# Performance work log

Measured on AMD Instinct MI355X. Metric: run time of the kernel, lower is better.

## Reference

```python
import jax, jax.numpy as jnp
import numpy as np

B, N_NUC, N_UP, N_DOWN = 512, 16, 32, 32
N_ELEC = N_UP + N_DOWN            # 64 electrons
F = 8                             # edge feature dim (Gaussian RBF envelopes)
D = N_NUC * F                     # embedding_dim = 128 (positional electron embeddings)
L = 3                             # n_interactions
N_ATOM_TYPES = 4


def _rbf(diff):
    # diff: [..., 3] -> [..., F]; Gaussian RBF features of the interparticle distance
    d = jnp.sqrt(jnp.sum(diff * diff, axis=-1) + 1e-12)
    mu = jnp.linspace(0.0, 4.0, F, dtype=diff.dtype)
    return jnp.exp(-(d[..., None] - mu) ** 2)


def setup_inputs() -> dict:
    key = jax.random.key(0)
    ks = jax.random.split(key, 9)
    r = 2.0 * jax.random.normal(ks[0], (B, N_ELEC, 3), dtype=jnp.float32)
    R = 2.0 * jax.random.normal(ks[1], (B, N_NUC, 3), dtype=jnp.float32)
    atom_types = jax.random.randint(ks[2], (N_NUC,), 0, N_ATOM_TYPES)
    embed_table = 0.1 * jax.random.normal(ks[3], (N_ATOM_TYPES, D), dtype=jnp.float32)
    we_same = 0.1 * jax.random.normal(ks[4], (L, F, D), dtype=jnp.float32)
    we_anti = 0.1 * jax.random.normal(ks[5], (L, F, D), dtype=jnp.float32)
    we_ne = 0.1 * jax.random.normal(ks[6], (L, F, D), dtype=jnp.float32)
    w_up = 0.05 * jax.random.normal(ks[7], (L, 4 * D, D), dtype=jnp.float32)
    b_up = jnp.zeros((L, D), dtype=jnp.float32)
    return {
        'r': r, 'R': R, 'embed_table': embed_table,
        'we_same': we_same, 'we_anti': we_anti, 'we_ne': we_ne,
        'w_up': w_up, 'b_up': b_up, 'atom_types': atom_types,
    }


def reference(r, R, embed_table, we_same, we_anti, we_ne, w_up, b_up, atom_types):
    # --- molecular graph edge construction (pairwise differences + edge features) ---
    ee_feat = _rbf(r[:, :, None, :] - r[:, None, :, :])   # [B, e, e, F]
    ne_feat = _rbf(r[:, :, None, :] - R[:, None, :, :])   # [B, e, n, F]

    spin = jnp.arange(N_ELEC) >= N_UP
    eye = jnp.eye(N_ELEC, dtype=bool)
    same_m = ((spin[:, None] == spin[None, :]) & ~eye).astype(ee_feat.dtype)  # no self-interaction
    anti_m = (spin[:, None] != spin[None, :]).astype(ee_feat.dtype)
    feat_same = ee_feat * same_m[None, :, :, None]
    feat_anti = ee_feat * anti_m[None, :, :, None]

    # --- node factory: positional electron embeddings (dense scatter of ne features == reshape) ---
    x = ne_feat.reshape(ne_feat.shape[0], N_ELEC, N_NUC * F)  # [B, e, D]
    y = embed_table[atom_types]                               # [n, D] nuclei embeddings

    # --- message-passing layers ---
    for l in range(L):
        # messages = Linear(edge_feats) * sender embedding, summed over senders per receiver;
        # contract sender axis first to keep intermediates at [B, e, F, D]
        t_s = jnp.einsum('bijf,bjd->bifd', feat_same, x)
        z_s = jnp.einsum('bifd,fd->bid', t_s, we_same[l])
        t_a = jnp.einsum('bijf,bjd->bifd', feat_anti, x)
        z_a = jnp.einsum('bifd,fd->bid', t_a, we_anti[l])
        t_n = jnp.einsum('binf,nd->bifd', ne_feat, y)
        z_n = jnp.einsum('bifd,fd->bid', t_n, we_ne[l])
        upd = jnp.concatenate([x, z_s, z_a, z_n], axis=-1)    # [B, e, 4D]
        x = x + jnp.tanh(upd @ w_up[l] + b_up[l])
    return x  # final electron embeddings [B, N_ELEC, D]
```

## Files before the change

### kernel.cpp

```cpp
#include <hip/hip_runtime.h>


typedef unsigned short u16;
typedef unsigned int u32;
typedef __attribute__((ext_vector_type(8))) short short8;
typedef __attribute__((ext_vector_type(4))) float f32x4;
typedef __attribute__((ext_vector_type(4))) u32 u32x4;
typedef _Float16 h2 __attribute__((ext_vector_type(2)));

__device__ __forceinline__ u16 f2h(float f){ return __builtin_bit_cast(u16, (_Float16)f); }
__device__ __forceinline__ float h2f(u16 a){ return (float)__builtin_bit_cast(_Float16, a); }

__device__ __forceinline__ short8 rbf8(float dd){
  short8 a;
#pragma unroll
  for (int f = 0; f < 8; f++){
    float u = dd - (4.0f/7.0f)*(float)f;
    a[f] = (short)f2h(__expf(-u*u));
  }
  return a;
}

__global__ __launch_bounds__(256) void gnn_prep(
    const float* __restrict__ w_up, const float* __restrict__ we_ne,
    const float* __restrict__ embed, const int* __restrict__ atypes,
    u16* __restrict__ wsegs){
  __shared__ u16 lw[16384];
  const int blk = blockIdx.x;
  const int l = blk / 5, seg = blk % 5;
  const int tid = threadIdx.x;
  if (seg < 4){
    const float* src = w_up + (l*512 + seg*128)*128;
#pragma unroll
    for (int mm = 0; mm < 16; mm++){
      int idx = mm*1024 + tid*4;
      float4 v = *(const float4*)(src + idx);
      lw[idx+0] = f2h(v.x); lw[idx+1] = f2h(v.y);
      lw[idx+2] = f2h(v.z); lw[idx+3] = f2h(v.w);
    }
  } else {
#pragma unroll
    for (int mm = 0; mm < 16; mm++){
      int idx = mm*1024 + tid*4;
      int k = idx >> 7, dout = idx & 127;
      int n = k >> 3, f = k & 7;
      float4 ye = *(const float4*)(embed + atypes[n]*128 + dout);
      float4 wn = *(const float4*)(we_ne + (l*8 + f)*128 + dout);
      lw[idx+0] = f2h(ye.x*wn.x); lw[idx+1] = f2h(ye.y*wn.y);
      lw[idx+2] = f2h(ye.z*wn.z); lw[idx+3] = f2h(ye.w*wn.w);
    }
  }
  __syncthreads();
  u16* dst = wsegs + blk*16384;
  const int col = tid & 15, q = (tid >> 4) & 3;
#pragma unroll
  for (int m = 0; m < 8; m++){
    int slot = m*4 + (tid >> 6);
    int c = slot >> 3, nt = slot & 7;
    int kbase = c*32 + q*8;
    int dout = nt*16 + col;
    short8 vv;
#pragma unroll
    for (int jj = 0; jj < 8; jj++) vv[jj] = (short)lw[(kbase+jj)*128 + dout];
    *(short8*)(dst + m*2048 + tid*8) = vv;
  }
}

__global__ __launch_bounds__(256, 2) void gnn_main(
    const float* __restrict__ r_g, const float* __restrict__ R_g,
    const float* __restrict__ weS_g, const float* __restrict__ weA_g,
    const float* __restrict__ bup_g,
    const u16* __restrict__ wsegs,
    float* __restrict__ out)
{
  extern __shared__ __attribute__((aligned(16))) u16 lds[];
  u16* const wb  = lds;
  u16* const xb  = lds + 16384;
  u16* const zst = lds + 25088;

  const int tid  = threadIdx.x;
  const int lane = tid & 63;
  const int w    = tid >> 6;
  const int b    = blockIdx.x;
  const int col  = lane & 15;
  const int q    = lane >> 4;
  const int i0   = w * 16;
  const int sp   = w >> 1;
  const int mrow = i0 + col;
  const int loff = (q*16 + col) * 8;

  u32x4 stg[8];
  auto stg_ld = [&](const u16* src){
#pragma unroll
    for (int m = 0; m < 8; m++) stg[m] = *(const u32x4*)(src + m*2048 + tid*8);
  };
  auto stg_st = [&](u16* dst){
#pragma unroll
    for (int m = 0; m < 8; m++) *(u32x4*)(dst + m*2048 + tid*8) = stg[m];
  };
  auto gemm_seg = [&](const u16* wbuf, const u16* arows, f32x4* acc){
#pragma unroll
    for (int c = 0; c < 4; c++){
      short8 a = *(const short8*)(arows + mrow*136 + c*32 + (q<<3));
#pragma unroll
      for (int nt = 0; nt < 8; nt++){
        short8 bf = *(const short8*)(wbuf + c*4096 + nt*512 + loff);
        acc[nt] = __builtin_amdgcn_mfma_f32_16x16x32_f16(a, bf, acc[nt], 0, 0, 0);
      }
    }
  };

  short8 aS[8], aA[8];
  float dN[4];
  {
    float* rs = (float*)zst;
    float* Rs = rs + 256;
    if (tid < 64){
#pragma unroll
      for (int k = 0; k < 3; k++) rs[tid*4+k] = r_g[(b*64+tid)*3 + k];
    } else if (tid < 80){
      int n = tid - 64;
#pragma unroll
      for (int k = 0; k < 3; k++) Rs[n*4+k] = R_g[(b*16+n)*3 + k];
    }
    __syncthreads();
    {
      float x0 = rs[mrow*4], x1 = rs[mrow*4+1], x2 = rs[mrow*4+2];
#pragma unroll
      for (int c = 0; c < 8; c++){
        int j = 32*sp + 4*c + q;
        float dx = x0-rs[j*4], dy = x1-rs[j*4+1], dz = x2-rs[j*4+2];
        float dd = sqrtf(dx*dx + dy*dy + dz*dz + 1e-12f);
        aS[c] = rbf8(dd);
        if (j == mrow) aS[c] = (short8)0;
        j = 32*(1-sp) + 4*c + q;
        dx = x0-rs[j*4]; dy = x1-rs[j*4+1]; dz = x2-rs[j*4+2];
        aA[c] = rbf8(sqrtf(dx*dx + dy*dy + dz*dz + 1e-12f));
      }
#pragma unroll
      for (int c = 0; c < 4; c++){
        int n = 4*c + q;
        float dx = x0-Rs[n*4], dy = x1-Rs[n*4+1], dz = x2-Rs[n*4+2];
        dN[c] = sqrtf(dx*dx + dy*dy + dz*dz + 1e-12f);
      }
    }
    {
      int i = tid >> 2, nb = (tid & 3)*4;
      float y0 = rs[i*4], y1 = rs[i*4+1], y2 = rs[i*4+2];
#pragma unroll
      for (int nn = 0; nn < 4; nn++){
        int n = nb + nn;
        float dx = y0-Rs[n*4], dy = y1-Rs[n*4+1], dz = y2-Rs[n*4+2];
        float dd = sqrtf(dx*dx + dy*dy + dz*dz + 1e-12f);
        *(short8*)&xb[i*136 + n*8] = rbf8(dd);
      }
    }
    stg_ld(wsegs + 0);
    stg_st(wb);
    __syncthreads();
  }

  f32x4 xr[8];
#pragma unroll
  for (int nt = 0; nt < 8; nt++)
#pragma unroll
    for (int rr = 0; rr < 4; rr++)
      xr[nt][rr] = h2f(xb[(i0 + q*4 + rr)*136 + nt*16 + col]);

  const f32x4 vzero = {0.f, 0.f, 0.f, 0.f};

#pragma unroll 1
  for (int l = 0; l < 3; l++){
    const u16* slab = wsegs + l*81920;

    float bupr[8];
#pragma unroll
    for (int nt = 0; nt < 8; nt++) bupr[nt] = bup_g[l*128 + nt*16 + col];

    f32x4 upd[8];
#pragma unroll
    for (int nt = 0; nt < 8; nt++) upd[nt] = vzero;

    auto zpass = [&](int pass){
      const float* weX = pass ? weA_g : weS_g;
      const int jb0 = pass ? 32*(1-sp) : 32*sp;
      const short8* aF = pass ? aA : aS;
      f32x4 zacc[8];
#pragma unroll
      for (int nt = 0; nt < 8; nt++) zacc[nt] = vzero;
#pragma unroll
      for (int nt = 0; nt < 8; nt++){
        h2 wp[4];
#pragma unroll
        for (int p = 0; p < 4; p++){
          h2 t;
          t[0] = (_Float16)weX[(l*8 + 2*p  )*128 + nt*16 + col];
          t[1] = (_Float16)weX[(l*8 + 2*p+1)*128 + nt*16 + col];
          wp[p] = t;
        }
        u16 xv[8];
#pragma unroll
        for (int c = 0; c < 8; c++) xv[c] = xb[(jb0 + 4*c + q)*136 + nt*16 + col];
#pragma unroll
        for (int c = 0; c < 8; c++){
          _Float16 xh = __builtin_bit_cast(_Float16, xv[c]);
          h2 xd; xd[0] = xh; xd[1] = xh;
          u32x4 bu;
#pragma unroll
          for (int p = 0; p < 4; p++)
            bu[p] = __builtin_bit_cast(u32, (h2)(xd * wp[p]));
          short8 bf = __builtin_bit_cast(short8, bu);
          zacc[nt] = __builtin_amdgcn_mfma_f32_16x16x32_f16(aF[c], bf, zacc[nt], 0, 0, 0);
        }
      }
#pragma unroll
      for (int nt = 0; nt < 8; nt++)
#pragma unroll
        for (int rr = 0; rr < 4; rr++)
          zst[(i0 + q*4 + rr)*136 + nt*16 + col] = f2h(zacc[nt][rr]);
    };

    stg_ld(slab + 1*16384);
    zpass(0);
    gemm_seg(wb, xb, upd);
    __syncthreads();  stg_st(wb);  __syncthreads();
    stg_ld(slab + 2*16384);
    gemm_seg(wb, zst, upd);
    __syncthreads();  stg_st(wb);  __syncthreads();
    stg_ld(slab + 4*16384);
    zpass(1);
    gemm_seg(wb, zst, upd);
    __syncthreads();  stg_st(wb);  __syncthreads();
    stg_ld(slab + 3*16384);
    {
      f32x4 zn[8];
#pragma unroll
      for (int nt = 0; nt < 8; nt++) zn[nt] = vzero;
#pragma unroll
      for (int c = 0; c < 4; c++){
        short8 a = rbf8(dN[c]);
#pragma unroll
        for (int nt = 0; nt < 8; nt++){
          short8 bf = *(const short8*)(wb + c*4096 + nt*512 + loff);
          zn[nt] = __builtin_amdgcn_mfma_f32_16x16x32_f16(a, bf, zn[nt], 0, 0, 0);
        }
      }
#pragma unroll
      for (int nt = 0; nt < 8; nt++)
#pragma unroll
        for (int rr = 0; rr < 4; rr++)
          zst[(i0 + q*4 + rr)*136 + nt*16 + col] = f2h(zn[nt][rr]);
    }
    __syncthreads();  stg_st(wb);  __syncthreads();
    if (l < 2) stg_ld(slab + 81920);
    gemm_seg(wb, zst, upd);
#pragma unroll
    for (int nt = 0; nt < 8; nt++){
#pragma unroll
      for (int rr = 0; rr < 4; rr++){
        float v = upd[nt][rr] + bupr[nt];
        float e = __expf(2.0f * v);
        float th = 1.0f - 2.0f * __builtin_amdgcn_rcpf(e + 1.0f);
        xr[nt][rr] += th;
      }
    }
    if (l < 2){
#pragma unroll
      for (int nt = 0; nt < 8; nt++)
#pragma unroll
        for (int rr = 0; rr < 4; rr++)
          xb[(i0 + q*4 + rr)*136 + nt*16 + col] = f2h(xr[nt][rr]);
      __syncthreads();  stg_st(wb);  __syncthreads();
    } else {
#pragma unroll
      for (int nt = 0; nt < 8; nt++)
#pragma unroll
        for (int rr = 0; rr < 4; rr++)
          out[(b*64 + i0 + q*4 + rr)*128 + nt*16 + col] = xr[nt][rr];
    }
  }
}

extern "C" void kernel_launch(void* const* d_in, const int* in_sizes, int n_in,
                              void* d_out, int out_size, void* d_ws, size_t ws_size,
                              hipStream_t stream){
  const float* r     = (const float*)d_in[0];
  const float* R     = (const float*)d_in[1];
  const float* embed = (const float*)d_in[2];
  const float* weS   = (const float*)d_in[3];
  const float* weA   = (const float*)d_in[4];
  const float* weN   = (const float*)d_in[5];
  const float* wup   = (const float*)d_in[6];
  const float* bup   = (const float*)d_in[7];
  const int* atyp    = (const int*)d_in[8];

  u16* wsegs = (u16*)d_ws;

  (void)hipFuncSetAttribute((const void*)gnn_main,
                            hipFuncAttributeMaxDynamicSharedMemorySize, 67584);
  gnn_prep<<<15, 256, 0, stream>>>(wup, weN, embed, atyp, wsegs);
  gnn_main<<<512, 256, 67584, stream>>>(r, R, weS, weA, bup, wsegs, (float*)d_out);
}
```

Before: 134.5 us.

## Split each row tile's output columns across two waves using 512-thread blocks

Doubles the block to 512 threads (8 waves). Each pair of waves now shares a 16-row tile and each wave computes half of the 128 output columns (4 of 8 n-tiles). This halves the accumulator and staging registers per wave and spreads each batch element's work over more waves to improve latency hiding. A barrier is added after the anti-spin z pass because z rows are now written by two waves. The cost is more block-wide synchronisation, and the edge-feature A fragments are recomputed redundantly in both waves of each pair.

Result: slower. 183.2 us (+36.2%).

```diff
diff --git a/kernel.cpp b/kernel.cpp
--- a/kernel.cpp
+++ b/kernel.cpp
@@ -66,7 +66,7 @@
   }
 }
 
-__global__ __launch_bounds__(256, 2) void gnn_main(
+__global__ __launch_bounds__(512, 4) void gnn_main(
     const float* __restrict__ r_g, const float* __restrict__ R_g,
     const float* __restrict__ weS_g, const float* __restrict__ weA_g,
     const float* __restrict__ bup_g,
@@ -81,30 +81,33 @@
   const int tid  = threadIdx.x;
   const int lane = tid & 63;
   const int w    = tid >> 6;
+  const int wq   = w >> 1;
+  const int wc   = w & 1;
   const int b    = blockIdx.x;
   const int col  = lane & 15;
   const int q    = lane >> 4;
-  const int i0   = w * 16;
-  const int sp   = w >> 1;
+  const int i0   = wq * 16;
+  const int sp   = wq >> 1;
   const int mrow = i0 + col;
   const int loff = (q*16 + col) * 8;
-
-  u32x4 stg[8];
+  const int ntb  = wc * 4;
+
+  u32x4 stg[4];
   auto stg_ld = [&](const u16* src){
 #pragma unroll
-    for (int m = 0; m < 8; m++) stg[m] = *(const u32x4*)(src + m*2048 + tid*8);
+    for (int m = 0; m < 4; m++) stg[m] = *(const u32x4*)(src + m*4096 + tid*8);
   };
   auto stg_st = [&](u16* dst){
 #pragma unroll
-    for (int m = 0; m < 8; m++) *(u32x4*)(dst + m*2048 + tid*8) = stg[m];
+    for (int m = 0; m < 4; m++) *(u32x4*)(dst + m*4096 + tid*8) = stg[m];
   };
   auto gemm_seg = [&](const u16* wbuf, const u16* arows, f32x4* acc){
 #pragma unroll
     for (int c = 0; c < 4; c++){
       short8 a = *(const short8*)(arows + mrow*136 + c*32 + (q<<3));
 #pragma unroll
-      for (int nt = 0; nt < 8; nt++){
-        short8 bf = *(const short8*)(wbuf + c*4096 + nt*512 + loff);
+      for (int nt = 0; nt < 4; nt++){
+        short8 bf = *(const short8*)(wbuf + c*4096 + (ntb+nt)*512 + loff);
         acc[nt] = __builtin_amdgcn_mfma_f32_16x16x32_f16(a, bf, acc[nt], 0, 0, 0);
       }
     }
@@ -145,10 +148,10 @@
       }
     }
     {
-      int i = tid >> 2, nb = (tid & 3)*4;
+      int i = tid >> 3, nb = (tid & 7)*2;
       float y0 = rs[i*4], y1 = rs[i*4+1], y2 = rs[i*4+2];
 #pragma unroll
-      for (int nn = 0; nn < 4; nn++){
+      for (int nn = 0; nn < 2; nn++){
         int n = nb + nn;
         float dx = y0-Rs[n*4], dy = y1-Rs[n*4+1], dz = y2-Rs[n*4+2];
         float dd = sqrtf(dx*dx + dy*dy + dz*dz + 1e-12f);
@@ -160,12 +163,12 @@
     __syncthreads();
   }
 
-  f32x4 xr[8];
-#pragma unroll
-  for (int nt = 0; nt < 8; nt++)
+  f32x4 xr[4];
+#pragma unroll
+  for (int nt = 0; nt < 4; nt++)
 #pragma unroll
     for (int rr = 0; rr < 4; rr++)
-      xr[nt][rr] = h2f(xb[(i0 + q*4 + rr)*136 + nt*16 + col]);
+      xr[nt][rr] = h2f(xb[(i0 + q*4 + rr)*136 + (ntb+nt)*16 + col]);
 
   const f32x4 vzero = {0.f, 0.f, 0.f, 0.f};
 
@@ -173,34 +176,35 @@
   for (int l = 0; l < 3; l++){
     const u16* slab = wsegs + l*81920;
 
-    float bupr[8];
-#pragma unroll
-    for (int nt = 0; nt < 8; nt++) bupr[nt] = bup_g[l*128 + nt*16 + col];
-
-    f32x4 upd[8];
-#pragma unroll
-    for (int nt = 0; nt < 8; nt++) upd[nt] = vzero;
+    float bupr[4];
+#pragma unroll
+    for (int nt = 0; nt < 4; nt++) bupr[nt] = bup_g[l*128 + (ntb+nt)*16 + col];
+
+    f32x4 upd[4];
+#pragma unroll
+    for (int nt = 0; nt < 4; nt++) upd[nt] = vzero;
 
     auto zpass = [&](int pass){
       const float* weX = pass ? weA_g : weS_g;
       const int jb0 = pass ? 32*(1-sp) : 32*sp;
       const short8* aF = pass ? aA : aS;
-      f32x4 zacc[8];
-#pragma unroll
-      for (int nt = 0; nt < 8; nt++) zacc[nt] = vzero;
-#pragma unroll
-      for (int nt = 0; nt < 8; nt++){
+      f32x4 zacc[4];
+#pragma unroll
+      for (int nt = 0; nt < 4; nt++) zacc[nt] = vzero;
+#pragma unroll
+      for (int nt = 0; nt < 4; nt++){
+        const int ntg = ntb + nt;
         h2 wp[4];
 #pragma unroll
         for (int p = 0; p < 4; p++){
           h2 t;
-          t[0] = (_Float16)weX[(l*8 + 2*p  )*128 + nt*16 + col];
-          t[1] = (_Float16)weX[(l*8 + 2*p+1)*128 + nt*16 + col];
+          t[0] = (_Float16)weX[(l*8 + 2*p  )*128 + ntg*16 + col];
+          t[1] = (_Float16)weX[(l*8 + 2*p+1)*128 + ntg*16 + col];
           wp[p] = t;
         }
         u16 xv[8];
 #pragma unroll
-        for (int c = 0; c < 8; c++) xv[c] = xb[(jb0 + 4*c + q)*136 + nt*16 + col];
+        for (int c = 0; c < 8; c++) xv[c] = xb[(jb0 + 4*c + q)*136 + ntg*16 + col];
 #pragma unroll
         for (int c = 0; c < 8; c++){
           _Float16 xh = __builtin_bit_cast(_Float16, xv[c]);
@@ -214,10 +218,10 @@
         }
       }
 #pragma unroll
-      for (int nt = 0; nt < 8; nt++)
+      for (int nt = 0; nt < 4; nt++)
 #pragma unroll
         for (int rr = 0; rr < 4; rr++)
-          zst[(i0 + q*4 + rr)*136 + nt*16 + col] = f2h(zacc[nt][rr]);
+          zst[(i0 + q*4 + rr)*136 + (ntb+nt)*16 + col] = f2h(zacc[nt][rr]);
     };
 
     stg_ld(slab + 1*16384);
@@ -229,33 +233,34 @@
     __syncthreads();  stg_st(wb);  __syncthreads();
     stg_ld(slab + 4*16384);
     zpass(1);
+    __syncthreads();
     gemm_seg(wb, zst, upd);
     __syncthreads();  stg_st(wb);  __syncthreads();
     stg_ld(slab + 3*16384);
     {
-      f32x4 zn[8];
-#pragma unroll
-      for (int nt = 0; nt < 8; nt++) zn[nt] = vzero;
+      f32x4 zn[4];
+#pragma unroll
+      for (int nt = 0; nt < 4; nt++) zn[nt] = vzero;
 #pragma unroll
       for (int c = 0; c < 4; c++){
         short8 a = rbf8(dN[c]);
 #pragma unroll
-        for (int nt = 0; nt < 8; nt++){
-          short8 bf = *(const short8*)(wb + c*4096 + nt*512 + loff);
+        for (int nt = 0; nt < 4; nt++){
+          short8 bf = *(const short8*)(wb + c*4096 + (ntb+nt)*512 + loff);
           zn[nt] = __builtin_amdgcn_mfma_f32_16x16x32_f16(a, bf, zn[nt], 0, 0, 0);
         }
       }
 #pragma unroll
-      for (int nt = 0; nt < 8; nt++)
+      for (int nt = 0; nt < 4; nt++)
 #pragma unroll
         for (int rr = 0; rr < 4; rr++)
-          zst[(i0 + q*4 + rr)*136 + nt*16 + col] = f2h(zn[nt][rr]);
+          zst[(i0 + q*4 + rr)*136 + (ntb+nt)*16 + col] = f2h(zn[nt][rr]);
     }
     __syncthreads();  stg_st(wb);  __syncthreads();
     if (l < 2) stg_ld(slab + 81920);
     gemm_seg(wb, zst, upd);
 #pragma unroll
-    for (int nt = 0; nt < 8; nt++){
+    for (int nt = 0; nt < 4; nt++){
 #pragma unroll
       for (int rr = 0; rr < 4; rr++){
         float v = upd[nt][rr] + bupr[nt];
@@ -266,17 +271,17 @@
     }
     if (l < 2){
 #pragma unroll
-      for (int nt = 0; nt < 8; nt++)
+      for (int nt = 0; nt < 4; nt++)
 #pragma unroll
         for (int rr = 0; rr < 4; rr++)
-          xb[(i0 + q*4 + rr)*136 + nt*16 + col] = f2h(xr[nt][rr]);
+          xb[(i0 + q*4 + rr)*136 + (ntb+nt)*16 + col] = f2h(xr[nt][rr]);
       __syncthreads();  stg_st(wb);  __syncthreads();
     } else {
 #pragma unroll
-      for (int nt = 0; nt < 8; nt++)
+      for (int nt = 0; nt < 4; nt++)
 #pragma unroll
         for (int rr = 0; rr < 4; rr++)
-          out[(b*64 + i0 + q*4 + rr)*128 + nt*16 + col] = xr[nt][rr];
+          out[(b*64 + i0 + q*4 + rr)*128 + (ntb+nt)*16 + col] = xr[nt][rr];
     }
   }
 }
@@ -299,5 +304,5 @@
   (void)hipFuncSetAttribute((const void*)gnn_main,
                             hipFuncAttributeMaxDynamicSharedMemorySize, 67584);
   gnn_prep<<<15, 256, 0, stream>>>(wup, weN, embed, atyp, wsegs);
-  gnn_main<<<512, 256, 67584, stream>>>(r, R, weS, weA, bup, wsegs, (float*)d_out);
+  gnn_main<<<512, 512, 67584, stream>>>(r, R, weS, weA, bup, wsegs, (float*)d_out);
 }
```

## Read weight fragments directly from global memory instead of LDS staging

Applied to the files above, without the earlier changes.

Removes the register-staged copy of each packed weight segment into LDS and the paired barriers around it. The MFMA B-fragments are now loaded straight from the global workspace, which every block shares and so should mostly hit in L2. This roughly halves the dynamic LDS footprint and cuts the number of __syncthreads per layer. The trade-off is that global-load latency now sits directly in the MFMA inner loops, with no explicit prefetch to hide it.

Measured after the change: 142.5 us. +6.0%, slower.

```diff
diff --git a/kernel.cpp b/kernel.cpp
--- a/kernel.cpp
+++ b/kernel.cpp
@@ -74,9 +74,10 @@
     float* __restrict__ out)
 {
   extern __shared__ __attribute__((aligned(16))) u16 lds[];
-  u16* const wb  = lds;
-  u16* const xb  = lds + 16384;
-  u16* const zst = lds + 25088;
+  u16* const xb  = lds;
+  u16* const zst = lds + 8704;
+  float* const rs = (float*)(lds + 17408);
+  float* const Rs = rs + 256;
 
   const int tid  = threadIdx.x;
   const int lane = tid & 63;
@@ -89,22 +90,13 @@
   const int mrow = i0 + col;
   const int loff = (q*16 + col) * 8;
 
-  u32x4 stg[8];
-  auto stg_ld = [&](const u16* src){
-#pragma unroll
-    for (int m = 0; m < 8; m++) stg[m] = *(const u32x4*)(src + m*2048 + tid*8);
-  };
-  auto stg_st = [&](u16* dst){
-#pragma unroll
-    for (int m = 0; m < 8; m++) *(u32x4*)(dst + m*2048 + tid*8) = stg[m];
-  };
-  auto gemm_seg = [&](const u16* wbuf, const u16* arows, f32x4* acc){
+  auto gemm_seg = [&](const u16* wseg_g, const u16* arows, f32x4* acc){
 #pragma unroll
     for (int c = 0; c < 4; c++){
       short8 a = *(const short8*)(arows + mrow*136 + c*32 + (q<<3));
 #pragma unroll
       for (int nt = 0; nt < 8; nt++){
-        short8 bf = *(const short8*)(wbuf + c*4096 + nt*512 + loff);
+        short8 bf = *(const short8*)(wseg_g + c*4096 + nt*512 + loff);
         acc[nt] = __builtin_amdgcn_mfma_f32_16x16x32_f16(a, bf, acc[nt], 0, 0, 0);
       }
     }
@@ -113,8 +105,6 @@
   short8 aS[8], aA[8];
   float dN[4];
   {
-    float* rs = (float*)zst;
-    float* Rs = rs + 256;
     if (tid < 64){
 #pragma unroll
       for (int k = 0; k < 3; k++) rs[tid*4+k] = r_g[(b*64+tid)*3 + k];
@@ -155,8 +145,6 @@
         *(short8*)&xb[i*136 + n*8] = rbf8(dd);
       }
     }
-    stg_ld(wsegs + 0);
-    stg_st(wb);
     __syncthreads();
   }
 
@@ -172,10 +160,6 @@
 #pragma unroll 1
   for (int l = 0; l < 3; l++){
     const u16* slab = wsegs + l*81920;
-
-    float bupr[8];
-#pragma unroll
-    for (int nt = 0; nt < 8; nt++) bupr[nt] = bup_g[l*128 + nt*16 + col];
 
     f32x4 upd[8];
 #pragma unroll
@@ -220,19 +204,13 @@
           zst[(i0 + q*4 + rr)*136 + nt*16 + col] = f2h(zacc[nt][rr]);
     };
 
-    stg_ld(slab + 1*16384);
     zpass(0);
-    gemm_seg(wb, xb, upd);
-    __syncthreads();  stg_st(wb);  __syncthreads();
-    stg_ld(slab + 2*16384);
-    gemm_seg(wb, zst, upd);
-    __syncthreads();  stg_st(wb);  __syncthreads();
-    stg_ld(slab + 4*16384);
+    gemm_seg(slab + 0*16384, xb,  upd);
+    gemm_seg(slab + 1*16384, zst, upd);
     zpass(1);
-    gemm_seg(wb, zst, upd);
-    __syncthreads();  stg_st(wb);  __syncthreads();
-    stg_ld(slab + 3*16384);
-    {
+    gemm_seg(slab + 2*16384, zst, upd);
+    {
+      const u16* yseg = slab + 4*16384;
       f32x4 zn[8];
 #pragma unroll
       for (int nt = 0; nt < 8; nt++) zn[nt] = vzero;
@@ -241,7 +219,7 @@
         short8 a = rbf8(dN[c]);
 #pragma unroll
         for (int nt = 0; nt < 8; nt++){
-          short8 bf = *(const short8*)(wb + c*4096 + nt*512 + loff);
+          short8 bf = *(const short8*)(yseg + c*4096 + nt*512 + loff);
           zn[nt] = __builtin_amdgcn_mfma_f32_16x16x32_f16(a, bf, zn[nt], 0, 0, 0);
         }
       }
@@ -251,17 +229,21 @@
         for (int rr = 0; rr < 4; rr++)
           zst[(i0 + q*4 + rr)*136 + nt*16 + col] = f2h(zn[nt][rr]);
     }
-    __syncthreads();  stg_st(wb);  __syncthreads();
-    if (l < 2) stg_ld(slab + 81920);
-    gemm_seg(wb, zst, upd);
-#pragma unroll
-    for (int nt = 0; nt < 8; nt++){
-#pragma unroll
-      for (int rr = 0; rr < 4; rr++){
-        float v = upd[nt][rr] + bupr[nt];
-        float e = __expf(2.0f * v);
-        float th = 1.0f - 2.0f * __builtin_amdgcn_rcpf(e + 1.0f);
-        xr[nt][rr] += th;
+    gemm_seg(slab + 3*16384, zst, upd);
+
+    {
+      float bupr[8];
+#pragma unroll
+      for (int nt = 0; nt < 8; nt++) bupr[nt] = bup_g[l*128 + nt*16 + col];
+#pragma unroll
+      for (int nt = 0; nt < 8; nt++){
+#pragma unroll
+        for (int rr = 0; rr < 4; rr++){
+          float v = upd[nt][rr] + bupr[nt];
+          float e = __expf(2.0f * v);
+          float th = 1.0f - 2.0f * __builtin_amdgcn_rcpf(e + 1.0f);
+          xr[nt][rr] += th;
+        }
       }
     }
     if (l < 2){
@@ -270,7 +252,7 @@
 #pragma unroll
         for (int rr = 0; rr < 4; rr++)
           xb[(i0 + q*4 + rr)*136 + nt*16 + col] = f2h(xr[nt][rr]);
-      __syncthreads();  stg_st(wb);  __syncthreads();
+      __syncthreads();
     } else {
 #pragma unroll
       for (int nt = 0; nt < 8; nt++)
@@ -297,7 +279,7 @@
   u16* wsegs = (u16*)d_ws;
 
   (void)hipFuncSetAttribute((const void*)gnn_main,
-                            hipFuncAttributeMaxDynamicSharedMemorySize, 67584);
+                            hipFuncAttributeMaxDynamicSharedMemorySize, 36096);
   gnn_prep<<<15, 256, 0, stream>>>(wup, weN, embed, atyp, wsegs);
-  gnn_main<<<512, 256, 67584, stream>>>(r, R, weS, weA, bup, wsegs, (float*)d_out);
-}
+  gnn_main<<<512, 256, 36096, stream>>>(r, R, weS, weA, bup, wsegs, (float*)d_out);
+}
```
